# Optimization experiments

Hardware: AMD Instinct MI355X
Metric: run time of the kernel (lower is better)

## Reference

```python
import jax, jax.numpy as jnp
import numpy as np
from jax import nn as jnn

N = 100000      # nodes
E = 3200000     # edges (avg degree 32)
G = 1024        # graphs in batch
F_IN = 3        # num_features (hard-coded in module)
D = 32          # dim (hard-coded in module)
BN_EPS = 1e-5


def setup_inputs() -> dict:
    key = jax.random.key(0)
    ks = jax.random.split(key, 24)
    def lin(k, i, o):
        return (jax.random.normal(k, (i, o), jnp.float32) / np.sqrt(i)).astype(jnp.float32)
    inp = {}
    inp["x"] = jax.random.normal(ks[0], (N, F_IN), jnp.float32)
    inp["edge_index"] = jax.random.randint(ks[1], (2, E), 0, N, dtype=jnp.int32)
    inp["batch"] = jnp.sort(jax.random.randint(ks[2], (N,), 0, G, dtype=jnp.int32))
    idx = 3
    in_dims = [F_IN, D, D]
    for l in (1, 2, 3):
        inp[f"W{l}a"] = lin(ks[idx], in_dims[l - 1], D); idx += 1
        inp[f"b{l}a"] = jnp.zeros((D,), jnp.float32)
        inp[f"W{l}b"] = lin(ks[idx], D, D); idx += 1
        inp[f"b{l}b"] = jnp.zeros((D,), jnp.float32)
        inp[f"g{l}"] = jnp.ones((D,), jnp.float32)            # BN gamma
        inp[f"be{l}"] = jnp.zeros((D,), jnp.float32)          # BN beta
        inp[f"m{l}"] = 0.1 * jax.random.normal(ks[idx], (D,), jnp.float32); idx += 1  # running mean
        inp[f"v{l}"] = jax.random.uniform(ks[idx], (D,), jnp.float32, 0.5, 1.5); idx += 1  # running var
    inp["Wf1"] = lin(ks[idx], D, D); idx += 1
    inp["bf1"] = jnp.zeros((D,), jnp.float32)
    inp["Wf2"] = lin(ks[idx], D, 1)
    inp["bf2"] = jnp.zeros((1,), jnp.float32)
    return inp


def reference(x, edge_index, batch,
              W1a, b1a, W1b, b1b, g1, be1, m1, v1,
              W2a, b2a, W2b, b2b, g2, be2, m2, v2,
              W3a, b3a, W3b, b3b, g3, be3, m3, v3,
              Wf1, bf1, Wf2, bf2):
    src, dst = edge_index[0], edge_index[1]

    def gin_bn(h, Wa, ba, Wb, bb, g, be, m, v):
        # GINConv (eps=0): nn(x + sum_{j->i} x_j); then relu; then BatchNorm1d (eval stats)
        agg = jax.ops.segment_sum(h[src], dst, num_segments=N) + h  # [N, d]
        h2 = jnn.relu(agg @ Wa + ba) @ Wb + bb                      # 2-layer MLP
        h2 = jnn.relu(h2)
        return g * (h2 - m) * jax.lax.rsqrt(v + BN_EPS) + be

    h = gin_bn(x, W1a, b1a, W1b, b1b, g1, be1, m1, v1)
    h = gin_bn(h, W2a, b2a, W2b, b2b, g2, be2, m2, v2)
    h = gin_bn(h, W3a, b3a, W3b, b3b, g3, be3, m3, v3)
    p = jax.ops.segment_sum(h, batch, num_segments=G)   # global_add_pool -> [G, D]
    p = jnn.relu(p @ Wf1 + bf1)
    # dropout p=0.5 is identity at inference
    return jnp.tanh(p @ Wf2 + bf2)                      # [G, 1]
```

## Files before the change

kernel.cpp:

```cpp
#include <hip/hip_runtime.h>
#include <math.h>

#define D 32
#define BN_EPS 1e-5f
#define NRANGE 512
#define RWC 196
#define MAXD 80
#define EPB 8192
#define K1_TPB 512
#define EPT (EPB / K1_TPB)
#define PCH 8

__global__ __launch_bounds__(K1_TPB) void build_part(
    const int* __restrict__ src, const int* __restrict__ dst,
    unsigned int* __restrict__ part, int* __restrict__ gcount,
    int E, int cap, int RW, unsigned long long M) {
    __shared__ unsigned int sorted[EPB];
    __shared__ unsigned short rid[EPB];
    __shared__ int cnt[NRANGE];
    __shared__ int exc[NRANGE];
    __shared__ int cur[NRANGE];
    __shared__ int gbase[NRANGE];
    int t = threadIdx.x;
    cnt[t] = 0;
    __syncthreads();

    int base = blockIdx.x * EPB;
    int n = min(EPB, E - base);

    unsigned int mypk[EPT];
    unsigned short myr[EPT];
#pragma unroll
    for (int k = 0; k < EPT; k++) {
        int i = t + k * K1_TPB;
        if (i < n) {
            int d = dst[base + i];
            int s = src[base + i];
            int r = (int)(((unsigned long long)d * M) >> 40);
            mypk[k] = ((unsigned)(d - r * RW) << 17) | (unsigned)s;
            myr[k] = (unsigned short)r;
            atomicAdd(&cnt[r], 1);
        } else myr[k] = 0xFFFFu;
    }
    __syncthreads();

    int inc = cnt[t];
    exc[t] = inc;
    __syncthreads();
    for (int s = 1; s < NRANGE; s <<= 1) {
        int u = (t >= s) ? exc[t - s] : 0;
        __syncthreads();
        exc[t] += u;
        __syncthreads();
    }
    int excl = exc[t] - cnt[t];
    __syncthreads();
    exc[t] = excl;
    cur[t] = excl;
    gbase[t] = atomicAdd(&gcount[t], cnt[t]);
    __syncthreads();

#pragma unroll
    for (int k = 0; k < EPT; k++) {
        if (myr[k] != 0xFFFFu) {
            int j = atomicAdd(&cur[myr[k]], 1);
            sorted[j] = mypk[k];
            rid[j] = myr[k];
        }
    }
    __syncthreads();

    for (int j = t; j < n; j += K1_TPB) {
        int r = rid[j];
        int pos = gbase[r] + (j - exc[r]);
        if (pos < cap) part[(size_t)r * cap + pos] = sorted[j];
    }
}

__global__ __launch_bounds__(1024) void build_csr(
    const unsigned int* __restrict__ part, const int* __restrict__ gcount,
    int* __restrict__ col, int* __restrict__ deg,
    int cap, int RW, int N, int maxd) {
    __shared__ int bucket[RWC * MAXD];
    __shared__ int rank_[RWC];
    int r = blockIdx.x, t = threadIdx.x, T = blockDim.x;
    for (int i = t; i < RW; i += T) rank_[i] = 0;
    __syncthreads();

    int count = gcount[r]; if (count > cap) count = cap;
    const unsigned int* p = part + (size_t)r * cap;
    for (int i = t; i < count; i += T) {
        unsigned int v = p[i];
        int dl = (int)(v >> 17);
        int s = (int)(v & 0x1FFFFu);
        int slot = atomicAdd(&rank_[dl], 1);
        if (slot < maxd) bucket[dl * maxd + slot] = s;
    }
    __syncthreads();

    int nbase = r * RW;
    int nvalid = N - nbase; if (nvalid > RW) nvalid = RW;
    if (nvalid <= 0) return;
    int words = nvalid * maxd;
    int4* dst4 = (int4*)&col[(size_t)nbase * maxd];
    const int4* src4 = (const int4*)bucket;
    int nq = words >> 2;
    for (int i = t; i < nq; i += T) dst4[i] = src4[i];
    for (int i = t; i < nvalid; i += T) {
        int rk = rank_[i];
        deg[nbase + i] = rk < maxd ? rk : maxd;
    }
}

__global__ void compute_y(const float* __restrict__ x, const float* __restrict__ W1a,
                          float* __restrict__ y, int N) {
    long long gid = (long long)blockIdx.x * blockDim.x + threadIdx.x;
    int i = (int)(gid >> 5);
    int lane = (int)(gid & 31);
    if (i >= N) return;
    float x0 = x[i * 3 + 0], x1 = x[i * 3 + 1], x2 = x[i * 3 + 2];
    float t = x0 * W1a[0 * D + lane];
    t = fmaf(x1, W1a[1 * D + lane], t);
    t = fmaf(x2, W1a[2 * D + lane], t);
    y[(size_t)i * D + lane] = t;
}

template <bool SKIP_WA>
__global__ void layer_fused(const float* __restrict__ hin, const int* __restrict__ deg,
                            const int* __restrict__ col, int maxd,
                            const float* __restrict__ Wa, const float* __restrict__ ba,
                            const float* __restrict__ Wb, const float* __restrict__ bb,
                            const float* __restrict__ g, const float* __restrict__ be,
                            const float* __restrict__ m, const float* __restrict__ v,
                            float* __restrict__ hout, int N) {
    long long gid = (long long)blockIdx.x * blockDim.x + threadIdx.x;
    int i = (int)(gid >> 5);
    int lane = (int)(gid & 31);
    if (i >= N) return;

    float acc = hin[(size_t)i * D + lane];
    int dg = deg[i];
    if (dg > maxd) dg = maxd;
    const int* cp = &col[(size_t)i * maxd];
    int e = 0;
    for (; e + 16 <= dg; e += 16) {
        int4 c0 = *(const int4*)&cp[e];
        int4 c1 = *(const int4*)&cp[e + 4];
        int4 c2 = *(const int4*)&cp[e + 8];
        int4 c3 = *(const int4*)&cp[e + 12];
        float a0 = hin[(size_t)c0.x * D + lane];
        float a1 = hin[(size_t)c0.y * D + lane];
        float a2 = hin[(size_t)c0.z * D + lane];
        float a3 = hin[(size_t)c0.w * D + lane];
        float a4 = hin[(size_t)c1.x * D + lane];
        float a5 = hin[(size_t)c1.y * D + lane];
        float a6 = hin[(size_t)c1.z * D + lane];
        float a7 = hin[(size_t)c1.w * D + lane];
        float a8 = hin[(size_t)c2.x * D + lane];
        float a9 = hin[(size_t)c2.y * D + lane];
        float aa = hin[(size_t)c2.z * D + lane];
        float ab = hin[(size_t)c2.w * D + lane];
        float ac = hin[(size_t)c3.x * D + lane];
        float ad = hin[(size_t)c3.y * D + lane];
        float ae = hin[(size_t)c3.z * D + lane];
        float af = hin[(size_t)c3.w * D + lane];
        acc += ((a0 + a1) + (a2 + a3)) + ((a4 + a5) + (a6 + a7)) +
               (((a8 + a9) + (aa + ab)) + ((ac + ad) + (ae + af)));
    }
    for (; e + 4 <= dg; e += 4) {
        int4 c = *(const int4*)&cp[e];
        float a0 = hin[(size_t)c.x * D + lane];
        float a1 = hin[(size_t)c.y * D + lane];
        float a2 = hin[(size_t)c.z * D + lane];
        float a3 = hin[(size_t)c.w * D + lane];
        acc += (a0 + a1) + (a2 + a3);
    }
    for (; e < dg; e++) acc += hin[(size_t)cp[e] * D + lane];

    float t;
    if (SKIP_WA) {
        t = fmaxf(acc + ba[lane], 0.f);
    } else {
        t = ba[lane];
#pragma unroll
        for (int k = 0; k < D; k++) {
            float ak = __shfl(acc, k, D);
            t = fmaf(ak, Wa[k * D + lane], t);
        }
        t = fmaxf(t, 0.f);
    }
    float o = bb[lane];
#pragma unroll
    for (int j = 0; j < D; j++) {
        float tj = __shfl(t, j, D);
        o = fmaf(tj, Wb[j * D + lane], o);
    }
    o = fmaxf(o, 0.f);
    hout[(size_t)i * D + lane] =
        g[lane] * (o - m[lane]) * rsqrtf(v[lane] + BN_EPS) + be[lane];
}

__device__ __forceinline__ int lower_bound_i(const int* a, int n, int key) {
    int lo = 0, hi = n;
    while (lo < hi) {
        int mid = (lo + hi) >> 1;
        if (a[mid] < key) lo = mid + 1; else hi = mid;
    }
    return lo;
}

__global__ void pool_partial(const float* __restrict__ h, const int* __restrict__ batch,
                             float* __restrict__ pool, int N, int G) {
    long long gid = (long long)blockIdx.x * blockDim.x + threadIdx.x;
    int grp = (int)(gid >> 5);
    int lane = (int)(gid & 31);
    int gi = grp / PCH;
    int c = grp - gi * PCH;
    if (gi >= G) return;
    int lo = lower_bound_i(batch, N, gi);
    int hi = lower_bound_i(batch, N, gi + 1);
    int len = hi - lo;
    if (len <= 0) return;
    int chunk = (len + PCH - 1) / PCH;
    int s = lo + c * chunk;
    int e = s + chunk; if (e > hi) e = hi;
    if (s >= e) return;
    float p = 0.f;
    for (int n = s; n < e; n++) p += h[(size_t)n * D + lane];
    atomicAdd(&pool[(size_t)gi * D + lane], p);
}

__global__ void head_kernel(const float* __restrict__ pool, const float* __restrict__ Wf1,
                            const float* __restrict__ bf1, const float* __restrict__ Wf2,
                            const float* __restrict__ bf2, float* __restrict__ out, int G) {
    long long gid = (long long)blockIdx.x * blockDim.x + threadIdx.x;
    int gi = (int)(gid >> 5);
    int lane = (int)(gid & 31);
    if (gi >= G) return;
    float p = pool[(size_t)gi * D + lane];
    float q = bf1[lane];
#pragma unroll
    for (int j = 0; j < D; j++) {
        float pj = __shfl(p, j, D);
        q = fmaf(pj, Wf1[j * D + lane], q);
    }
    q = fmaxf(q, 0.f);
    float r = q * Wf2[lane];
#pragma unroll
    for (int off = 16; off; off >>= 1) r += __shfl_xor(r, off, D);
    if (lane == 0) out[gi] = tanhf(r + bf2[0]);
}

extern "C" void kernel_launch(void* const* d_in, const int* in_sizes, int n_in,
                              void* d_out, int out_size, void* d_ws, size_t ws_size,
                              hipStream_t stream) {
    const float* x = (const float*)d_in[0];
    const int* ei = (const int*)d_in[1];
    const int* batch = (const int*)d_in[2];
    const int E = in_sizes[1] / 2;
    const int N = in_sizes[2];
    const int G = out_size;
    const int* src = ei;
    const int* dst = ei + E;

    const float* P[3][8];
    for (int l = 0; l < 3; l++)
        for (int k = 0; k < 8; k++) P[l][k] = (const float*)d_in[3 + 8 * l + k];
    const float* Wf1 = (const float*)d_in[27];
    const float* bf1 = (const float*)d_in[28];
    const float* Wf2 = (const float*)d_in[29];
    const float* bf2 = (const float*)d_in[30];

    const int RW = (N + NRANGE - 1) / NRANGE;
    const unsigned long long M = ((1ull << 40) + RW - 1) / RW;
    int mean = (E + NRANGE - 1) / NRANGE;
    int cap = mean + mean / 8 + 64;
    cap = (cap + 7) & ~7;

    float* ws = (float*)d_ws;
    size_t off = 0;
    float* h0 = ws + off; off += (size_t)N * D;
    float* h1 = ws + off; off += (size_t)N * D;
    unsigned int* part = (unsigned int*)h0;
    int* deg = (int*)(ws + off); off += N;
    int* gcount = (int*)(ws + off); off += NRANGE;
    float* pool = ws + off; off += (size_t)G * D;
    int* col = (int*)(ws + off);
    size_t remaining = ws_size / 4 > off ? ws_size / 4 - off : 0;
    int maxd = (int)(remaining / (size_t)N);
    if (maxd > MAXD) maxd = MAXD;
    maxd &= ~3;
    if (maxd < 4) maxd = 4;

    const int B = 256;
    long long tN32 = (long long)N * D;
    int nbp = (E + EPB - 1) / EPB;

    hipMemsetAsync(gcount, 0, NRANGE * sizeof(int), stream);
    build_part<<<nbp, K1_TPB, 0, stream>>>(src, dst, part, gcount, E, cap, RW, M);
    build_csr<<<NRANGE, 1024, 0, stream>>>(part, gcount, col, deg, cap, RW, N, maxd);

    compute_y<<<(int)((tN32 + B - 1) / B), B, 0, stream>>>(x, P[0][0], h0, N);
    layer_fused<true><<<(int)((tN32 + B - 1) / B), B, 0, stream>>>(
        h0, deg, col, maxd, P[0][0], P[0][1], P[0][2], P[0][3],
        P[0][4], P[0][5], P[0][6], P[0][7], h1, N);

    layer_fused<false><<<(int)((tN32 + B - 1) / B), B, 0, stream>>>(
        h1, deg, col, maxd, P[1][0], P[1][1], P[1][2], P[1][3],
        P[1][4], P[1][5], P[1][6], P[1][7], h0, N);

    layer_fused<false><<<(int)((tN32 + B - 1) / B), B, 0, stream>>>(
        h0, deg, col, maxd, P[2][0], P[2][1], P[2][2], P[2][3],
        P[2][4], P[2][5], P[2][6], P[2][7], h1, N);

    hipMemsetAsync(pool, 0, (size_t)G * D * sizeof(float), stream);
    pool_partial<<<(int)(((long long)G * PCH * 32 + B - 1) / B), B, 0, stream>>>(
        h1, batch, pool, N, G);
    head_kernel<<<(int)(((long long)G * D + B - 1) / B), B, 0, stream>>>(
        pool, Wf1, bf1, Wf2, bf2, (float*)d_out, G);
}
```

Before: 375.3 us.

## Fuse CSR construction into each layer via per-block shared-memory bucket sort

Removes the separate build_csr kernel and the padded global column array. Each layer kernel now reloads its node range's edge partition and counting-sorts it into LDS, then gathers neighbors from the LDS column list. This avoids writing and re-reading a large padded adjacency array and drops the max-degree truncation. The cost is redoing the sort in every layer and launching far fewer, larger blocks. The build_part edge-per-block size is also halved, and the partition buffer gets its own workspace region instead of sharing h0.

```diff
diff --git a/kernel.cpp b/kernel.cpp
--- a/kernel.cpp
+++ b/kernel.cpp
@@ -4,9 +4,10 @@
 #define D 32
 #define BN_EPS 1e-5f
 #define NRANGE 512
-#define RWC 196
-#define MAXD 80
-#define EPB 8192
+#define RWB 256
+#define SCAP 8192
+#define EPTL 7
+#define EPB 4096
 #define K1_TPB 512
 #define EPT (EPB / K1_TPB)
 #define PCH 8
@@ -77,41 +78,6 @@
     }
 }
 
-__global__ __launch_bounds__(1024) void build_csr(
-    const unsigned int* __restrict__ part, const int* __restrict__ gcount,
-    int* __restrict__ col, int* __restrict__ deg,
-    int cap, int RW, int N, int maxd) {
-    __shared__ int bucket[RWC * MAXD];
-    __shared__ int rank_[RWC];
-    int r = blockIdx.x, t = threadIdx.x, T = blockDim.x;
-    for (int i = t; i < RW; i += T) rank_[i] = 0;
-    __syncthreads();
-
-    int count = gcount[r]; if (count > cap) count = cap;
-    const unsigned int* p = part + (size_t)r * cap;
-    for (int i = t; i < count; i += T) {
-        unsigned int v = p[i];
-        int dl = (int)(v >> 17);
-        int s = (int)(v & 0x1FFFFu);
-        int slot = atomicAdd(&rank_[dl], 1);
-        if (slot < maxd) bucket[dl * maxd + slot] = s;
-    }
-    __syncthreads();
-
-    int nbase = r * RW;
-    int nvalid = N - nbase; if (nvalid > RW) nvalid = RW;
-    if (nvalid <= 0) return;
-    int words = nvalid * maxd;
-    int4* dst4 = (int4*)&col[(size_t)nbase * maxd];
-    const int4* src4 = (const int4*)bucket;
-    int nq = words >> 2;
-    for (int i = t; i < nq; i += T) dst4[i] = src4[i];
-    for (int i = t; i < nvalid; i += T) {
-        int rk = rank_[i];
-        deg[nbase + i] = rk < maxd ? rk : maxd;
-    }
-}
-
 __global__ void compute_y(const float* __restrict__ x, const float* __restrict__ W1a,
                           float* __restrict__ y, int N) {
     long long gid = (long long)blockIdx.x * blockDim.x + threadIdx.x;
@@ -126,78 +92,130 @@
 }
 
 template <bool SKIP_WA>
-__global__ void layer_fused(const float* __restrict__ hin, const int* __restrict__ deg,
-                            const int* __restrict__ col, int maxd,
-                            const float* __restrict__ Wa, const float* __restrict__ ba,
-                            const float* __restrict__ Wb, const float* __restrict__ bb,
-                            const float* __restrict__ g, const float* __restrict__ be,
-                            const float* __restrict__ m, const float* __restrict__ v,
-                            float* __restrict__ hout, int N) {
-    long long gid = (long long)blockIdx.x * blockDim.x + threadIdx.x;
-    int i = (int)(gid >> 5);
-    int lane = (int)(gid & 31);
-    if (i >= N) return;
-
-    float acc = hin[(size_t)i * D + lane];
-    int dg = deg[i];
-    if (dg > maxd) dg = maxd;
-    const int* cp = &col[(size_t)i * maxd];
-    int e = 0;
-    for (; e + 16 <= dg; e += 16) {
-        int4 c0 = *(const int4*)&cp[e];
-        int4 c1 = *(const int4*)&cp[e + 4];
-        int4 c2 = *(const int4*)&cp[e + 8];
-        int4 c3 = *(const int4*)&cp[e + 12];
-        float a0 = hin[(size_t)c0.x * D + lane];
-        float a1 = hin[(size_t)c0.y * D + lane];
-        float a2 = hin[(size_t)c0.z * D + lane];
-        float a3 = hin[(size_t)c0.w * D + lane];
-        float a4 = hin[(size_t)c1.x * D + lane];
-        float a5 = hin[(size_t)c1.y * D + lane];
-        float a6 = hin[(size_t)c1.z * D + lane];
-        float a7 = hin[(size_t)c1.w * D + lane];
-        float a8 = hin[(size_t)c2.x * D + lane];
-        float a9 = hin[(size_t)c2.y * D + lane];
-        float aa = hin[(size_t)c2.z * D + lane];
-        float ab = hin[(size_t)c2.w * D + lane];
-        float ac = hin[(size_t)c3.x * D + lane];
-        float ad = hin[(size_t)c3.y * D + lane];
-        float ae = hin[(size_t)c3.z * D + lane];
-        float af = hin[(size_t)c3.w * D + lane];
-        acc += ((a0 + a1) + (a2 + a3)) + ((a4 + a5) + (a6 + a7)) +
-               (((a8 + a9) + (aa + ab)) + ((ac + ad) + (ae + af)));
-    }
-    for (; e + 4 <= dg; e += 4) {
-        int4 c = *(const int4*)&cp[e];
-        float a0 = hin[(size_t)c.x * D + lane];
-        float a1 = hin[(size_t)c.y * D + lane];
-        float a2 = hin[(size_t)c.z * D + lane];
-        float a3 = hin[(size_t)c.w * D + lane];
-        acc += (a0 + a1) + (a2 + a3);
-    }
-    for (; e < dg; e++) acc += hin[(size_t)cp[e] * D + lane];
-
-    float t;
-    if (SKIP_WA) {
-        t = fmaxf(acc + ba[lane], 0.f);
-    } else {
-        t = ba[lane];
-#pragma unroll
-        for (int k = 0; k < D; k++) {
-            float ak = __shfl(acc, k, D);
-            t = fmaf(ak, Wa[k * D + lane], t);
-        }
-        t = fmaxf(t, 0.f);
-    }
-    float o = bb[lane];
-#pragma unroll
-    for (int j = 0; j < D; j++) {
-        float tj = __shfl(t, j, D);
-        o = fmaf(tj, Wb[j * D + lane], o);
-    }
-    o = fmaxf(o, 0.f);
-    hout[(size_t)i * D + lane] =
-        g[lane] * (o - m[lane]) * rsqrtf(v[lane] + BN_EPS) + be[lane];
+__global__ __launch_bounds__(1024) void layer_sorted(
+    const float* __restrict__ hin, const unsigned int* __restrict__ part,
+    const int* __restrict__ gcount, int cap, int RW, int N,
+    const float* __restrict__ Wa, const float* __restrict__ ba,
+    const float* __restrict__ Wb, const float* __restrict__ bb,
+    const float* __restrict__ g, const float* __restrict__ be,
+    const float* __restrict__ m, const float* __restrict__ v,
+    float* __restrict__ hout) {
+    __shared__ unsigned int scol[SCAP];
+    __shared__ int cnt[RWB];
+    __shared__ int base_[RWB];
+    __shared__ int cur[RWB];
+    int r = blockIdx.x;
+    int t = threadIdx.x;
+    if (t < RWB) cnt[t] = 0;
+    __syncthreads();
+
+    int count = gcount[r]; if (count > cap) count = cap;
+    const unsigned int* p = part + (size_t)r * cap;
+
+    unsigned int myv[EPTL];
+#pragma unroll
+    for (int k = 0; k < EPTL; k++) {
+        int i = t + k * 1024;
+        myv[k] = 0xFFFFFFFFu;
+        if (i < count) {
+            myv[k] = p[i];
+            atomicAdd(&cnt[myv[k] >> 17], 1);
+        }
+    }
+    __syncthreads();
+
+    int pc = (t < RWB) ? ((cnt[t] + 3) & ~3) : 0;
+    if (t < RWB) base_[t] = pc;
+    __syncthreads();
+    for (int s = 1; s < RWB; s <<= 1) {
+        int u = 0;
+        if (t < RWB && t >= s) u = base_[t - s];
+        __syncthreads();
+        if (t < RWB) base_[t] += u;
+        __syncthreads();
+    }
+    if (t < RWB) {
+        int excl = base_[t] - pc;
+        base_[t] = excl;
+        cur[t] = excl;
+    }
+    __syncthreads();
+
+#pragma unroll
+    for (int k = 0; k < EPTL; k++) {
+        if (myv[k] != 0xFFFFFFFFu) {
+            int dl = (int)(myv[k] >> 17);
+            int j = atomicAdd(&cur[dl], 1);
+            scol[j] = myv[k] & 0x1FFFFu;
+        }
+    }
+    __syncthreads();
+
+    int gidx = t >> 5, lane = t & 31;
+    int nbase = r * RW;
+    for (int nl = gidx; nl < RW; nl += 32) {
+        int node = nbase + nl;
+        if (node >= N) continue;
+        float acc = hin[(size_t)node * D + lane];
+        int dg = cnt[nl];
+        int bs = base_[nl];
+        int e = 0;
+        for (; e + 16 <= dg; e += 16) {
+            uint4 c0 = *(const uint4*)&scol[bs + e];
+            uint4 c1 = *(const uint4*)&scol[bs + e + 4];
+            uint4 c2 = *(const uint4*)&scol[bs + e + 8];
+            uint4 c3 = *(const uint4*)&scol[bs + e + 12];
+            float a0 = hin[(size_t)c0.x * D + lane];
+            float a1 = hin[(size_t)c0.y * D + lane];
+            float a2 = hin[(size_t)c0.z * D + lane];
+            float a3 = hin[(size_t)c0.w * D + lane];
+            float a4 = hin[(size_t)c1.x * D + lane];
+            float a5 = hin[(size_t)c1.y * D + lane];
+            float a6 = hin[(size_t)c1.z * D + lane];
+            float a7 = hin[(size_t)c1.w * D + lane];
+            float a8 = hin[(size_t)c2.x * D + lane];
+            float a9 = hin[(size_t)c2.y * D + lane];
+            float aa = hin[(size_t)c2.z * D + lane];
+            float ab = hin[(size_t)c2.w * D + lane];
+            float ac = hin[(size_t)c3.x * D + lane];
+            float ad = hin[(size_t)c3.y * D + lane];
+            float ae = hin[(size_t)c3.z * D + lane];
+            float af = hin[(size_t)c3.w * D + lane];
+            acc += ((a0 + a1) + (a2 + a3)) + ((a4 + a5) + (a6 + a7)) +
+                   (((a8 + a9) + (aa + ab)) + ((ac + ad) + (ae + af)));
+        }
+        for (; e + 4 <= dg; e += 4) {
+            uint4 c = *(const uint4*)&scol[bs + e];
+            float a0 = hin[(size_t)c.x * D + lane];
+            float a1 = hin[(size_t)c.y * D + lane];
+            float a2 = hin[(size_t)c.z * D + lane];
+            float a3 = hin[(size_t)c.w * D + lane];
+            acc += (a0 + a1) + (a2 + a3);
+        }
+        for (; e < dg; e++) acc += hin[(size_t)scol[bs + e] * D + lane];
+
+        float tv;
+        if (SKIP_WA) {
+            tv = fmaxf(acc + ba[lane], 0.f);
+        } else {
+            tv = ba[lane];
+#pragma unroll
+            for (int k = 0; k < D; k++) {
+                float ak = __shfl(acc, k, D);
+                tv = fmaf(ak, Wa[k * D + lane], tv);
+            }
+            tv = fmaxf(tv, 0.f);
+        }
+        float o = bb[lane];
+#pragma unroll
+        for (int j = 0; j < D; j++) {
+            float tj = __shfl(tv, j, D);
+            o = fmaf(tj, Wb[j * D + lane], o);
+        }
+        o = fmaxf(o, 0.f);
+        hout[(size_t)node * D + lane] =
+            g[lane] * (o - m[lane]) * rsqrtf(v[lane] + BN_EPS) + be[lane];
+    }
 }
 
 __device__ __forceinline__ int lower_bound_i(const int* a, int n, int key) {
@@ -281,16 +299,9 @@
     size_t off = 0;
     float* h0 = ws + off; off += (size_t)N * D;
     float* h1 = ws + off; off += (size_t)N * D;
-    unsigned int* part = (unsigned int*)h0;
-    int* deg = (int*)(ws + off); off += N;
+    unsigned int* part = (unsigned int*)(ws + off); off += (size_t)NRANGE * cap;
     int* gcount = (int*)(ws + off); off += NRANGE;
     float* pool = ws + off; off += (size_t)G * D;
-    int* col = (int*)(ws + off);
-    size_t remaining = ws_size / 4 > off ? ws_size / 4 - off : 0;
-    int maxd = (int)(remaining / (size_t)N);
-    if (maxd > MAXD) maxd = MAXD;
-    maxd &= ~3;
-    if (maxd < 4) maxd = 4;
 
     const int B = 256;
     long long tN32 = (long long)N * D;
@@ -298,20 +309,19 @@
 
     hipMemsetAsync(gcount, 0, NRANGE * sizeof(int), stream);
     build_part<<<nbp, K1_TPB, 0, stream>>>(src, dst, part, gcount, E, cap, RW, M);
-    build_csr<<<NRANGE, 1024, 0, stream>>>(part, gcount, col, deg, cap, RW, N, maxd);
 
     compute_y<<<(int)((tN32 + B - 1) / B), B, 0, stream>>>(x, P[0][0], h0, N);
-    layer_fused<true><<<(int)((tN32 + B - 1) / B), B, 0, stream>>>(
-        h0, deg, col, maxd, P[0][0], P[0][1], P[0][2], P[0][3],
-        P[0][4], P[0][5], P[0][6], P[0][7], h1, N);
-
-    layer_fused<false><<<(int)((tN32 + B - 1) / B), B, 0, stream>>>(
-        h1, deg, col, maxd, P[1][0], P[1][1], P[1][2], P[1][3],
-        P[1][4], P[1][5], P[1][6], P[1][7], h0, N);
-
-    layer_fused<false><<<(int)((tN32 + B - 1) / B), B, 0, stream>>>(
-        h0, deg, col, maxd, P[2][0], P[2][1], P[2][2], P[2][3],
-        P[2][4], P[2][5], P[2][6], P[2][7], h1, N);
+    layer_sorted<true><<<NRANGE, 1024, 0, stream>>>(
+        h0, part, gcount, cap, RW, N, P[0][0], P[0][1], P[0][2], P[0][3],
+        P[0][4], P[0][5], P[0][6], P[0][7], h1);
+
+    layer_sorted<false><<<NRANGE, 1024, 0, stream>>>(
+        h1, part, gcount, cap, RW, N, P[1][0], P[1][1], P[1][2], P[1][3],
+        P[1][4], P[1][5], P[1][6], P[1][7], h0);
+
+    layer_sorted<false><<<NRANGE, 1024, 0, stream>>>(
+        h0, part, gcount, cap, RW, N, P[2][0], P[2][1], P[2][2], P[2][3],
+        P[2][4], P[2][5], P[2][6], P[2][7], h1);
 
     hipMemsetAsync(pool, 0, (size_t)G * D * sizeof(float), stream);
     pool_partial<<<(int)(((long long)G * PCH * 32 + B - 1) / B), B, 0, stream>>>(
```

Result: slower. 399.3 us (+6.4%).

## Replace global-atomic edge partitioning with per-block sorted chunks and transposed metadata

Applied to the files above, without the earlier changes.

The edge bucketing no longer reserves slots in fixed-capacity global partitions through global atomics. Each block now writes its locally range-sorted chunk in place and records per-range counts and offsets. A small tiled transpose kernel reorders that metadata by range, and the CSR builder walks each block's segment for its range. This removes the global atomic contention and the capacity truncation, and halves the edges per block. In exchange it adds a launch, and the CSR builder does short serial, poorly coalesced reads per source block.

```diff
diff --git a/kernel.cpp b/kernel.cpp
--- a/kernel.cpp
+++ b/kernel.cpp
@@ -6,21 +6,20 @@
 #define NRANGE 512
 #define RWC 196
 #define MAXD 80
-#define EPB 8192
+#define EPB 4096
 #define K1_TPB 512
 #define EPT (EPB / K1_TPB)
 #define PCH 8
-
-__global__ __launch_bounds__(K1_TPB) void build_part(
+#define TD 32
+
+__global__ __launch_bounds__(K1_TPB) void build_part2(
     const int* __restrict__ src, const int* __restrict__ dst,
-    unsigned int* __restrict__ part, int* __restrict__ gcount,
-    int E, int cap, int RW, unsigned long long M) {
+    unsigned int* __restrict__ part2, int* __restrict__ cntA, int* __restrict__ offA,
+    int E, int RW, unsigned long long M) {
     __shared__ unsigned int sorted[EPB];
-    __shared__ unsigned short rid[EPB];
     __shared__ int cnt[NRANGE];
     __shared__ int exc[NRANGE];
     __shared__ int cur[NRANGE];
-    __shared__ int gbase[NRANGE];
     int t = threadIdx.x;
     cnt[t] = 0;
     __syncthreads();
@@ -57,7 +56,8 @@
     __syncthreads();
     exc[t] = excl;
     cur[t] = excl;
-    gbase[t] = atomicAdd(&gcount[t], cnt[t]);
+    cntA[(size_t)blockIdx.x * NRANGE + t] = cnt[t];
+    offA[(size_t)blockIdx.x * NRANGE + t] = excl;
     __syncthreads();
 
 #pragma unroll
@@ -65,36 +65,58 @@
         if (myr[k] != 0xFFFFu) {
             int j = atomicAdd(&cur[myr[k]], 1);
             sorted[j] = mypk[k];
-            rid[j] = myr[k];
-        }
-    }
-    __syncthreads();
-
-    for (int j = t; j < n; j += K1_TPB) {
-        int r = rid[j];
-        int pos = gbase[r] + (j - exc[r]);
-        if (pos < cap) part[(size_t)r * cap + pos] = sorted[j];
-    }
-}
-
-__global__ __launch_bounds__(1024) void build_csr(
-    const unsigned int* __restrict__ part, const int* __restrict__ gcount,
-    int* __restrict__ col, int* __restrict__ deg,
-    int cap, int RW, int N, int maxd) {
+        }
+    }
+    __syncthreads();
+
+    for (int j = t; j < n; j += K1_TPB) part2[(size_t)base + j] = sorted[j];
+}
+
+__global__ void transpose_meta(const int* __restrict__ cntA, const int* __restrict__ offA,
+                               int* __restrict__ cntT, int* __restrict__ offT, int nbp) {
+    __shared__ int ta[TD][TD + 1];
+    __shared__ int tb[TD][TD + 1];
+    int b0 = blockIdx.x * TD, r0 = blockIdx.y * TD;
+    int tx = threadIdx.x, ty = threadIdx.y;
+    for (int k = 0; k < TD; k += 8) {
+        int b = b0 + ty + k;
+        if (b < nbp) {
+            ta[ty + k][tx] = cntA[(size_t)b * NRANGE + r0 + tx];
+            tb[ty + k][tx] = offA[(size_t)b * NRANGE + r0 + tx];
+        }
+    }
+    __syncthreads();
+    for (int k = 0; k < TD; k += 8) {
+        int r = r0 + ty + k;
+        int b = b0 + tx;
+        if (b < nbp) {
+            cntT[(size_t)r * nbp + b] = ta[tx][ty + k];
+            offT[(size_t)r * nbp + b] = tb[tx][ty + k];
+        }
+    }
+}
+
+__global__ __launch_bounds__(1024) void build_csr2(
+    const unsigned int* __restrict__ part2, const int* __restrict__ cntT,
+    const int* __restrict__ offT, int* __restrict__ col, int* __restrict__ deg,
+    int nbp, int RW, int N, int maxd) {
     __shared__ int bucket[RWC * MAXD];
     __shared__ int rank_[RWC];
     int r = blockIdx.x, t = threadIdx.x, T = blockDim.x;
     for (int i = t; i < RW; i += T) rank_[i] = 0;
     __syncthreads();
 
-    int count = gcount[r]; if (count > cap) count = cap;
-    const unsigned int* p = part + (size_t)r * cap;
-    for (int i = t; i < count; i += T) {
-        unsigned int v = p[i];
-        int dl = (int)(v >> 17);
-        int s = (int)(v & 0x1FFFFu);
-        int slot = atomicAdd(&rank_[dl], 1);
-        if (slot < maxd) bucket[dl * maxd + slot] = s;
+    const int* cr = cntT + (size_t)r * nbp;
+    const int* orr = offT + (size_t)r * nbp;
+    for (int b = t; b < nbp; b += T) {
+        int c = cr[b];
+        const unsigned int* p = part2 + (size_t)b * EPB + orr[b];
+        for (int i = 0; i < c; i++) {
+            unsigned int v = p[i];
+            int dl = (int)(v >> 17);
+            int slot = atomicAdd(&rank_[dl], 1);
+            if (slot < maxd) bucket[dl * maxd + slot] = (int)(v & 0x1FFFFu);
+        }
     }
     __syncthreads();
 
@@ -273,18 +295,22 @@
 
     const int RW = (N + NRANGE - 1) / NRANGE;
     const unsigned long long M = ((1ull << 40) + RW - 1) / RW;
-    int mean = (E + NRANGE - 1) / NRANGE;
-    int cap = mean + mean / 8 + 64;
-    cap = (cap + 7) & ~7;
+    int nbp = (E + EPB - 1) / EPB;
+    size_t mcnt = (size_t)nbp * NRANGE;
 
     float* ws = (float*)d_ws;
     size_t off = 0;
     float* h0 = ws + off; off += (size_t)N * D;
     float* h1 = ws + off; off += (size_t)N * D;
-    unsigned int* part = (unsigned int*)h0;
+    unsigned int* part2 = (unsigned int*)h0;
+    size_t p2end = (size_t)nbp * EPB;
+    size_t moff = p2end > (size_t)N * D ? p2end : (size_t)N * D;
+    int* cntA = (int*)(ws + moff);
+    int* offA = cntA + mcnt;
+    int* cntT = offA + mcnt;
+    int* offT = cntT + mcnt;
+    float* pool = ws + off; off += (size_t)G * D;
     int* deg = (int*)(ws + off); off += N;
-    int* gcount = (int*)(ws + off); off += NRANGE;
-    float* pool = ws + off; off += (size_t)G * D;
     int* col = (int*)(ws + off);
     size_t remaining = ws_size / 4 > off ? ws_size / 4 - off : 0;
     int maxd = (int)(remaining / (size_t)N);
@@ -294,11 +320,11 @@
 
     const int B = 256;
     long long tN32 = (long long)N * D;
-    int nbp = (E + EPB - 1) / EPB;
-
-    hipMemsetAsync(gcount, 0, NRANGE * sizeof(int), stream);
-    build_part<<<nbp, K1_TPB, 0, stream>>>(src, dst, part, gcount, E, cap, RW, M);
-    build_csr<<<NRANGE, 1024, 0, stream>>>(part, gcount, col, deg, cap, RW, N, maxd);
+
+    build_part2<<<nbp, K1_TPB, 0, stream>>>(src, dst, part2, cntA, offA, E, RW, M);
+    transpose_meta<<<dim3((nbp + TD - 1) / TD, NRANGE / TD), dim3(TD, 8), 0, stream>>>(
+        cntA, offA, cntT, offT, nbp);
+    build_csr2<<<NRANGE, 1024, 0, stream>>>(part2, cntT, offT, col, deg, nbp, RW, N, maxd);
 
     compute_y<<<(int)((tN32 + B - 1) / B), B, 0, stream>>>(x, P[0][0], h0, N);
     layer_fused<true><<<(int)((tN32 + B - 1) / B), B, 0, stream>>>(
```

Measured after the change: 404.7 us. 1.08x slower.

## Aggregate raw 3-feature inputs in layer 1 and simplify edge partition bucketing

Applied to the files above, without the earlier changes.

Layer 1 no longer gathers 32-wide projected rows per edge. It packs x into float4 rows, sums the neighbours' raw 3 features, and applies W1a afterwards, using linearity to shrink gather traffic. The edge partition kernel drops its shared-memory prefix scan and sort in favour of fixed-capacity per-range shared buckets, with half the edges per block. This removes the scan barriers, but any bucket that receives more than 28 edges in a block silently drops the extra edges.

```diff
diff --git a/kernel.cpp b/kernel.cpp
--- a/kernel.cpp
+++ b/kernel.cpp
@@ -6,20 +6,17 @@
 #define NRANGE 512
 #define RWC 196
 #define MAXD 80
-#define EPB 8192
+#define EPB 4096
 #define K1_TPB 512
-#define EPT (EPB / K1_TPB)
+#define BCAP 28
 #define PCH 8
 
 __global__ __launch_bounds__(K1_TPB) void build_part(
     const int* __restrict__ src, const int* __restrict__ dst,
     unsigned int* __restrict__ part, int* __restrict__ gcount,
     int E, int cap, int RW, unsigned long long M) {
-    __shared__ unsigned int sorted[EPB];
-    __shared__ unsigned short rid[EPB];
+    __shared__ unsigned int bucket[NRANGE * BCAP];
     __shared__ int cnt[NRANGE];
-    __shared__ int exc[NRANGE];
-    __shared__ int cur[NRANGE];
     __shared__ int gbase[NRANGE];
     int t = threadIdx.x;
     cnt[t] = 0;
@@ -28,52 +25,28 @@
     int base = blockIdx.x * EPB;
     int n = min(EPB, E - base);
 
-    unsigned int mypk[EPT];
-    unsigned short myr[EPT];
-#pragma unroll
-    for (int k = 0; k < EPT; k++) {
-        int i = t + k * K1_TPB;
-        if (i < n) {
-            int d = dst[base + i];
-            int s = src[base + i];
-            int r = (int)(((unsigned long long)d * M) >> 40);
-            mypk[k] = ((unsigned)(d - r * RW) << 17) | (unsigned)s;
-            myr[k] = (unsigned short)r;
-            atomicAdd(&cnt[r], 1);
-        } else myr[k] = 0xFFFFu;
-    }
-    __syncthreads();
-
-    int inc = cnt[t];
-    exc[t] = inc;
-    __syncthreads();
-    for (int s = 1; s < NRANGE; s <<= 1) {
-        int u = (t >= s) ? exc[t - s] : 0;
-        __syncthreads();
-        exc[t] += u;
-        __syncthreads();
-    }
-    int excl = exc[t] - cnt[t];
-    __syncthreads();
-    exc[t] = excl;
-    cur[t] = excl;
-    gbase[t] = atomicAdd(&gcount[t], cnt[t]);
-    __syncthreads();
-
-#pragma unroll
-    for (int k = 0; k < EPT; k++) {
-        if (myr[k] != 0xFFFFu) {
-            int j = atomicAdd(&cur[myr[k]], 1);
-            sorted[j] = mypk[k];
-            rid[j] = myr[k];
+    for (int i = t; i < n; i += K1_TPB) {
+        int d = dst[base + i];
+        int s = src[base + i];
+        int r = (int)(((unsigned long long)d * M) >> 40);
+        int dl = d - r * RW;
+        int k = atomicAdd(&cnt[r], 1);
+        if (k < BCAP) bucket[r * BCAP + k] = ((unsigned)dl << 17) | (unsigned)s;
+    }
+    __syncthreads();
+
+    int c = cnt[t]; if (c > BCAP) c = BCAP;
+    gbase[t] = atomicAdd(&gcount[t], c);
+    __syncthreads();
+
+    for (int idx = t; idx < NRANGE * BCAP; idx += K1_TPB) {
+        int r = idx / BCAP;
+        int k = idx - r * BCAP;
+        int cr = cnt[r]; if (cr > BCAP) cr = BCAP;
+        if (k < cr) {
+            int pos = gbase[r] + k;
+            if (pos < cap) part[(size_t)r * cap + pos] = bucket[idx];
         }
-    }
-    __syncthreads();
-
-    for (int j = t; j < n; j += K1_TPB) {
-        int r = rid[j];
-        int pos = gbase[r] + (j - exc[r]);
-        if (pos < cap) part[(size_t)r * cap + pos] = sorted[j];
     }
 }
 
@@ -112,20 +85,66 @@
     }
 }
 
-__global__ void compute_y(const float* __restrict__ x, const float* __restrict__ W1a,
-                          float* __restrict__ y, int N) {
+__global__ void pack_x(const float* __restrict__ x, float4* __restrict__ xp, int N) {
+    int i = blockIdx.x * blockDim.x + threadIdx.x;
+    if (i >= N) return;
+    xp[i] = make_float4(x[3 * i], x[3 * i + 1], x[3 * i + 2], 0.f);
+}
+
+__global__ void layer1_direct(const float4* __restrict__ xp, const int* __restrict__ deg,
+                              const int* __restrict__ col, int maxd,
+                              const float* __restrict__ Wa, const float* __restrict__ ba,
+                              const float* __restrict__ Wb, const float* __restrict__ bb,
+                              const float* __restrict__ g, const float* __restrict__ be,
+                              const float* __restrict__ m, const float* __restrict__ v,
+                              float* __restrict__ hout, int N) {
     long long gid = (long long)blockIdx.x * blockDim.x + threadIdx.x;
     int i = (int)(gid >> 5);
     int lane = (int)(gid & 31);
     if (i >= N) return;
-    float x0 = x[i * 3 + 0], x1 = x[i * 3 + 1], x2 = x[i * 3 + 2];
-    float t = x0 * W1a[0 * D + lane];
-    t = fmaf(x1, W1a[1 * D + lane], t);
-    t = fmaf(x2, W1a[2 * D + lane], t);
-    y[(size_t)i * D + lane] = t;
-}
-
-template <bool SKIP_WA>
+
+    float4 sf = xp[i];
+    float s0 = sf.x, s1 = sf.y, s2 = sf.z;
+    int dg = deg[i];
+    if (dg > maxd) dg = maxd;
+    const int* cp = &col[(size_t)i * maxd];
+    int e = 0;
+    for (; e + 8 <= dg; e += 8) {
+        int4 c0 = *(const int4*)&cp[e];
+        int4 c1 = *(const int4*)&cp[e + 4];
+        float4 v0 = xp[c0.x];
+        float4 v1 = xp[c0.y];
+        float4 v2 = xp[c0.z];
+        float4 v3 = xp[c0.w];
+        float4 v4 = xp[c1.x];
+        float4 v5 = xp[c1.y];
+        float4 v6 = xp[c1.z];
+        float4 v7 = xp[c1.w];
+        s0 += ((v0.x + v1.x) + (v2.x + v3.x)) + ((v4.x + v5.x) + (v6.x + v7.x));
+        s1 += ((v0.y + v1.y) + (v2.y + v3.y)) + ((v4.y + v5.y) + (v6.y + v7.y));
+        s2 += ((v0.z + v1.z) + (v2.z + v3.z)) + ((v4.z + v5.z) + (v6.z + v7.z));
+    }
+    for (; e < dg; e++) {
+        float4 v0 = xp[cp[e]];
+        s0 += v0.x; s1 += v0.y; s2 += v0.z;
+    }
+
+    float t = ba[lane];
+    t = fmaf(s0, Wa[0 * D + lane], t);
+    t = fmaf(s1, Wa[1 * D + lane], t);
+    t = fmaf(s2, Wa[2 * D + lane], t);
+    t = fmaxf(t, 0.f);
+    float o = bb[lane];
+#pragma unroll
+    for (int j = 0; j < D; j++) {
+        float tj = __shfl(t, j, D);
+        o = fmaf(tj, Wb[j * D + lane], o);
+    }
+    o = fmaxf(o, 0.f);
+    hout[(size_t)i * D + lane] =
+        g[lane] * (o - m[lane]) * rsqrtf(v[lane] + BN_EPS) + be[lane];
+}
+
 __global__ void layer_fused(const float* __restrict__ hin, const int* __restrict__ deg,
                             const int* __restrict__ col, int maxd,
                             const float* __restrict__ Wa, const float* __restrict__ ba,
@@ -177,18 +196,13 @@
     }
     for (; e < dg; e++) acc += hin[(size_t)cp[e] * D + lane];
 
-    float t;
-    if (SKIP_WA) {
-        t = fmaxf(acc + ba[lane], 0.f);
-    } else {
-        t = ba[lane];
-#pragma unroll
-        for (int k = 0; k < D; k++) {
-            float ak = __shfl(acc, k, D);
-            t = fmaf(ak, Wa[k * D + lane], t);
-        }
-        t = fmaxf(t, 0.f);
-    }
+    float t = ba[lane];
+#pragma unroll
+    for (int k = 0; k < D; k++) {
+        float ak = __shfl(acc, k, D);
+        t = fmaf(ak, Wa[k * D + lane], t);
+    }
+    t = fmaxf(t, 0.f);
     float o = bb[lane];
 #pragma unroll
     for (int j = 0; j < D; j++) {
@@ -285,6 +299,7 @@
     int* deg = (int*)(ws + off); off += N;
     int* gcount = (int*)(ws + off); off += NRANGE;
     float* pool = ws + off; off += (size_t)G * D;
+    float4* xp = (float4*)(ws + off); off += (size_t)N * 4;
     int* col = (int*)(ws + off);
     size_t remaining = ws_size / 4 > off ? ws_size / 4 - off : 0;
     int maxd = (int)(remaining / (size_t)N);
@@ -300,16 +315,16 @@
     build_part<<<nbp, K1_TPB, 0, stream>>>(src, dst, part, gcount, E, cap, RW, M);
     build_csr<<<NRANGE, 1024, 0, stream>>>(part, gcount, col, deg, cap, RW, N, maxd);
 
-    compute_y<<<(int)((tN32 + B - 1) / B), B, 0, stream>>>(x, P[0][0], h0, N);
-    layer_fused<true><<<(int)((tN32 + B - 1) / B), B, 0, stream>>>(
-        h0, deg, col, maxd, P[0][0], P[0][1], P[0][2], P[0][3],
+    pack_x<<<(N + B - 1) / B, B, 0, stream>>>(x, xp, N);
+    layer1_direct<<<(int)((tN32 + B - 1) / B), B, 0, stream>>>(
+        xp, deg, col, maxd, P[0][0], P[0][1], P[0][2], P[0][3],
         P[0][4], P[0][5], P[0][6], P[0][7], h1, N);
 
-    layer_fused<false><<<(int)((tN32 + B - 1) / B), B, 0, stream>>>(
+    layer_fused<<<(int)((tN32 + B - 1) / B), B, 0, stream>>>(
         h1, deg, col, maxd, P[1][0], P[1][1], P[1][2], P[1][3],
         P[1][4], P[1][5], P[1][6], P[1][7], h0, N);
 
-    layer_fused<false><<<(int)((tN32 + B - 1) / B), B, 0, stream>>>(
+    layer_fused<<<(int)((tN32 + B - 1) / B), B, 0, stream>>>(
         h0, deg, col, maxd, P[2][0], P[2][1], P[2][2], P[2][3],
         P[2][4], P[2][5], P[2][6], P[2][7], h1, N);
 
```

New measurement: 403.1 us. 7.4% more time.
